# Kernel optimization log

Hardware: AMD Instinct MI355X
Metric: run time of the kernel (lower is better)

## Reference

```python
import jax, jax.numpy as jnp
import numpy as np

N_NODES = 40000
N_EDGES = 640000
N_FEAT = 128
HIDDEN = 128
N_GRAPHS = 64


def _sage_conv(x, src, dst, Wl, b, Wr):
    # PyG SAGEConv (aggr='mean', root_weight=True, normalize=False):
    # out_i = W_l @ mean_{j in N(i)} x_j + b + W_r @ x_i
    msg = x[src]                                             # [E, F]
    s = jax.ops.segment_sum(msg, dst, num_segments=N_NODES)  # [N, F]
    deg = jax.ops.segment_sum(jnp.ones((src.shape[0],), x.dtype), dst,
                              num_segments=N_NODES)
    agg = s / jnp.maximum(deg, 1.0)[:, None]
    return agg @ Wl + b + x @ Wr


def setup_inputs() -> dict:
    key = jax.random.key(0)
    ks = jax.random.split(key, 12)
    sc = 1.0 / np.sqrt(N_FEAT)
    x = jax.random.normal(ks[0], (N_NODES, N_FEAT), dtype=jnp.float32)
    edge_index = jax.random.randint(ks[1], (2, N_EDGES), 0, N_NODES, dtype=jnp.int32)
    batch = jnp.sort(jax.random.randint(ks[2], (N_NODES,), 0, N_GRAPHS, dtype=jnp.int32))
    mk = lambda k, shp: (jax.random.normal(k, shp, dtype=jnp.float32) * sc)
    return {
        'x': x, 'edge_index': edge_index, 'batch': batch,
        'W1l': mk(ks[3], (N_FEAT, HIDDEN)), 'b1': jnp.zeros((HIDDEN,), jnp.float32),
        'W1r': mk(ks[4], (N_FEAT, HIDDEN)),
        'W2l': mk(ks[5], (HIDDEN, HIDDEN)), 'b2': jnp.zeros((HIDDEN,), jnp.float32),
        'W2r': mk(ks[6], (HIDDEN, HIDDEN)),
        'W3l': mk(ks[7], (HIDDEN, HIDDEN)), 'b3': jnp.zeros((HIDDEN,), jnp.float32),
        'W3r': mk(ks[8], (HIDDEN, HIDDEN)),
        'Wlin': mk(ks[9], (3 * HIDDEN, HIDDEN)), 'blin': jnp.zeros((HIDDEN,), jnp.float32),
    }


def reference(x, edge_index, batch, W1l, b1, W1r, W2l, b2, W2r, W3l, b3, W3r, Wlin, blin):
    src, dst = edge_index[0], edge_index[1]
    h1 = jax.nn.relu(_sage_conv(x, src, dst, W1l, b1, W1r))
    h2 = jax.nn.relu(_sage_conv(h1, src, dst, W2l, b2, W2r))
    h3 = jax.nn.relu(_sage_conv(h2, src, dst, W3l, b3, W3r))
    h = jnp.concatenate([h1, h2, h3], axis=1)                # [N, 3*H]
    pooled = jax.ops.segment_sum(h, batch, num_segments=N_GRAPHS)  # global_add_pool
    out = jax.nn.relu(pooled @ Wlin + blin)                  # [G, H]
    return out
```

## Files before the change

### kernel.cpp

```cpp
#include <hip/hip_runtime.h>
#include <hip/hip_bf16.h>

#define N_NODES 40000
#define N_EDGES 640000
#define NFEAT 128
#define NGRAPHS 64
#define ECAP 1024

typedef __attribute__((ext_vector_type(8))) short short8;
typedef __attribute__((ext_vector_type(4))) float float4v;

static __device__ __forceinline__ float bf2f(unsigned short u) {
    unsigned int x = ((unsigned int)u) << 16;
    return __builtin_bit_cast(float, x);
}
static __device__ __forceinline__ unsigned short f2bf(float f) {
    unsigned int x = __builtin_bit_cast(unsigned int, f);
    unsigned int r = x + 0x7fffu + ((x >> 16) & 1u);
    return (unsigned short)(r >> 16);
}

__global__ void k_prep(const int* __restrict__ dst, int* __restrict__ deg,
                       const int* __restrict__ batch, int* __restrict__ goff,
                       const float* __restrict__ x, unsigned short* __restrict__ h0,
                       const float* __restrict__ Wl0, const float* __restrict__ Wr0,
                       const float* __restrict__ Wl1, const float* __restrict__ Wr1,
                       const float* __restrict__ Wl2, const float* __restrict__ Wr2,
                       unsigned short* __restrict__ Wt) {
    int b = blockIdx.x;
    if (b < 2500) {
        int e = b * 256 + threadIdx.x;
        if (e < N_EDGES) atomicAdd(&deg[dst[e]], 1);
    } else if (b < 2657) {
        int i = (b - 2500) * 256 + threadIdx.x;
        if (i >= N_NODES) return;
        int b1 = batch[i];
        int b0 = (i == 0) ? -1 : batch[i - 1];
        for (int g = b0 + 1; g <= b1; ++g) goff[g] = i;
        if (i == N_NODES - 1)
            for (int g = b1 + 1; g <= NGRAPHS; ++g) goff[g] = N_NODES;
    } else if (b < 12657) {
        int i = (b - 2657) * 256 + threadIdx.x;
        const int n = N_NODES * NFEAT / 2;
        if (i < n) {
            float a = x[2 * i], c = x[2 * i + 1];
            unsigned int u = (unsigned int)f2bf(a) | ((unsigned int)f2bf(c) << 16);
            ((unsigned int*)h0)[i] = u;
        }
    } else {
        int id = (b - 12657) * 256 + threadIdx.x;
        if (id >= 3 * 128 * 256) return;
        int l   = id >> 15;
        int rem = id & 32767;
        int nn  = rem >> 8;
        int k   = rem & 255;
        const float* Wl = (l == 0) ? Wl0 : (l == 1) ? Wl1 : Wl2;
        const float* Wr = (l == 0) ? Wr0 : (l == 1) ? Wr1 : Wr2;
        float v = (k < 128) ? Wl[k * 128 + nn] : Wr[(k - 128) * 128 + nn];
        Wt[id] = f2bf(v);
    }
}

__global__ __launch_bounds__(1024) void k_scan(const int* __restrict__ deg,
                                               int* __restrict__ offsets,
                                               int* __restrict__ cursor) {
    __shared__ int ws[16];
    __shared__ int s_boff;
    int tid = threadIdx.x;
    int b = blockIdx.x;
    int lane = tid & 63, wave = tid >> 6;

    int lim = b << 10;
    int s = 0;
    for (int i = tid; i < lim; i += 1024) s += deg[i];
    for (int d = 1; d < 64; d <<= 1) s += __shfl_xor(s, d, 64);
    if (lane == 0) ws[wave] = s;
    __syncthreads();
    if (tid == 0) {
        int t = 0;
        for (int w = 0; w < 16; ++w) t += ws[w];
        s_boff = t;
    }
    __syncthreads();
    int boff = s_boff;

    int i = (b << 10) + tid;
    int v = (i < N_NODES) ? deg[i] : 0;
    int incl = v;
    for (int d = 1; d < 64; d <<= 1) {
        int t = __shfl_up(incl, d, 64);
        if (lane >= d) incl += t;
    }
    __syncthreads();
    if (lane == 63) ws[wave] = incl;
    __syncthreads();
    if (wave == 0 && lane < 16) {
        int w = ws[lane];
        for (int d = 1; d < 16; d <<= 1) {
            int t = __shfl_up(w, d, 64);
            if (lane >= d) w += t;
        }
        ws[lane] = w;
    }
    __syncthreads();
    int waveOff = (wave == 0) ? 0 : ws[wave - 1];
    if (i < N_NODES) {
        int o = boff + waveOff + incl - v;
        offsets[i] = o;
        cursor[i]  = o;
    }
    if (b == 39 && tid == 0) offsets[N_NODES] = N_EDGES;
}

__global__ void k_fill(const int* __restrict__ src, const int* __restrict__ dst,
                       int* __restrict__ cursor, int* __restrict__ esrc) {
    int e = blockIdx.x * 256 + threadIdx.x;
    if (e < N_EDGES) {
        int d = dst[e];
        int p = atomicAdd(&cursor[d], 1);
        esrc[p] = src[e];
    }
}

__global__ __launch_bounds__(256, 7) void k_sage(
        const unsigned short* __restrict__ hin,
        const int* __restrict__ offsets,
        const int* __restrict__ esrc,
        const unsigned short* __restrict__ Wt,
        const float* __restrict__ bias,
        unsigned short* __restrict__ hout) {
    __shared__ __align__(16) unsigned short As[32][264];
    __shared__ int eidx[ECAP];
    int tid = threadIdx.x;
    int row0 = blockIdx.x * 32;

    int estart = offsets[row0];
    int ecnt   = offsets[row0 + 32] - estart;
    int staged = ecnt < ECAP ? ecnt : ECAP;

    for (int p = 0; p < 2; ++p) {
        int ci = tid + p * 256;
        int r = ci >> 4, c8 = ci & 15;
        uint4 v = *(const uint4*)(hin + (size_t)(row0 + r) * 128 + c8 * 8);
        *(uint4*)(&As[r][128 + c8 * 8]) = v;
    }
    for (int t = tid; t < staged; t += 256) eidx[t] = esrc[estart + t];
    __syncthreads();

    {
        int grp = tid >> 4;
        int sub = tid & 15;
        for (int nn = 0; nn < 2; ++nn) {
            int r = nn * 16 + grp;
            int node = row0 + r;
            int beg = offsets[node], end = offsets[node + 1];
            float a[8];
            for (int i = 0; i < 8; ++i) a[i] = 0.f;
            auto acc8 = [&](uint4 u) {
                a[0] += bf2f((unsigned short)(u.x & 0xffffu));
                a[1] += bf2f((unsigned short)(u.x >> 16));
                a[2] += bf2f((unsigned short)(u.y & 0xffffu));
                a[3] += bf2f((unsigned short)(u.y >> 16));
                a[4] += bf2f((unsigned short)(u.z & 0xffffu));
                a[5] += bf2f((unsigned short)(u.z >> 16));
                a[6] += bf2f((unsigned short)(u.w & 0xffffu));
                a[7] += bf2f((unsigned short)(u.w >> 16));
            };
            if (end - estart <= staged) {
                int lj = beg - estart, lend = end - estart;
                for (; lj + 8 <= lend; lj += 8) {
                    int s0 = eidx[lj],     s1 = eidx[lj + 1];
                    int s2 = eidx[lj + 2], s3 = eidx[lj + 3];
                    int s4 = eidx[lj + 4], s5 = eidx[lj + 5];
                    int s6 = eidx[lj + 6], s7 = eidx[lj + 7];
                    uint4 u0 = *(const uint4*)(hin + (size_t)s0 * 128 + sub * 8);
                    uint4 u1 = *(const uint4*)(hin + (size_t)s1 * 128 + sub * 8);
                    uint4 u2 = *(const uint4*)(hin + (size_t)s2 * 128 + sub * 8);
                    uint4 u3 = *(const uint4*)(hin + (size_t)s3 * 128 + sub * 8);
                    uint4 u4 = *(const uint4*)(hin + (size_t)s4 * 128 + sub * 8);
                    uint4 u5 = *(const uint4*)(hin + (size_t)s5 * 128 + sub * 8);
                    uint4 u6 = *(const uint4*)(hin + (size_t)s6 * 128 + sub * 8);
                    uint4 u7 = *(const uint4*)(hin + (size_t)s7 * 128 + sub * 8);
                    acc8(u0); acc8(u1); acc8(u2); acc8(u3);
                    acc8(u4); acc8(u5); acc8(u6); acc8(u7);
                }
                for (; lj < lend; ++lj) {
                    int s = eidx[lj];
                    uint4 u = *(const uint4*)(hin + (size_t)s * 128 + sub * 8);
                    acc8(u);
                }
            } else {
                for (int j = beg; j < end; ++j) {
                    int s = esrc[j];
                    uint4 u = *(const uint4*)(hin + (size_t)s * 128 + sub * 8);
                    acc8(u);
                }
            }
            int deg = end - beg;
            float inv = 1.f / (float)(deg > 1 ? deg : 1);
            uint4 v;
            v.x = (unsigned int)f2bf(a[0] * inv) | ((unsigned int)f2bf(a[1] * inv) << 16);
            v.y = (unsigned int)f2bf(a[2] * inv) | ((unsigned int)f2bf(a[3] * inv) << 16);
            v.z = (unsigned int)f2bf(a[4] * inv) | ((unsigned int)f2bf(a[5] * inv) << 16);
            v.w = (unsigned int)f2bf(a[6] * inv) | ((unsigned int)f2bf(a[7] * inv) << 16);
            *(uint4*)(&As[r][sub * 8]) = v;
        }
    }
    __syncthreads();

    int wave = tid >> 6, lane = tid & 63;
    int quad = lane >> 4, l16 = lane & 15;
    float4v acc[2][2];
    for (int rt = 0; rt < 2; ++rt)
        for (int ct = 0; ct < 2; ++ct) acc[rt][ct] = {0.f, 0.f, 0.f, 0.f};

    int ncol0 = wave * 32;
    for (int kc = 0; kc < 8; ++kc) {
        int k0 = kc * 32 + quad * 8;
        short8 a[2], b[2];
        for (int rt = 0; rt < 2; ++rt)
            a[rt] = *(const short8*)(&As[rt * 16 + l16][k0]);
        for (int ct = 0; ct < 2; ++ct)
            b[ct] = *(const short8*)(Wt + (size_t)(ncol0 + ct * 16 + l16) * 256 + k0);
        for (int rt = 0; rt < 2; ++rt)
            for (int ct = 0; ct < 2; ++ct)
                acc[rt][ct] = __builtin_amdgcn_mfma_f32_16x16x32_bf16(
                    a[rt], b[ct], acc[rt][ct], 0, 0, 0);
    }

    for (int ct = 0; ct < 2; ++ct) {
        int col = ncol0 + ct * 16 + l16;
        float bv = bias[col];
        for (int rt = 0; rt < 2; ++rt) {
            int r0 = rt * 16 + quad * 4;
            for (int i = 0; i < 4; ++i) {
                float v = acc[rt][ct][i] + bv;
                v = v > 0.f ? v : 0.f;
                hout[(size_t)(row0 + r0 + i) * 128 + col] = f2bf(v);
            }
        }
    }
}

__global__ __launch_bounds__(256) void k_pool(const unsigned short* __restrict__ h1,
                                              const unsigned short* __restrict__ h2,
                                              const unsigned short* __restrict__ h3,
                                              const int* __restrict__ goff,
                                              float* __restrict__ pooled) {
    __shared__ float red[4][16][8];
    int b = blockIdx.x;
    int g = b / 3, aidx = b % 3;
    const unsigned short* h = (aidx == 0) ? h1 : (aidx == 1) ? h2 : h3;
    int beg = goff[g], end = goff[g + 1];
    int tid = threadIdx.x;
    int rp = tid >> 4;
    int ch = tid & 15;
    float a[8];
    for (int i = 0; i < 8; ++i) a[i] = 0.f;
    for (int r = beg + rp; r < end; r += 16) {
        uint4 u = *(const uint4*)(h + (size_t)r * 128 + ch * 8);
        a[0] += bf2f((unsigned short)(u.x & 0xffffu));
        a[1] += bf2f((unsigned short)(u.x >> 16));
        a[2] += bf2f((unsigned short)(u.y & 0xffffu));
        a[3] += bf2f((unsigned short)(u.y >> 16));
        a[4] += bf2f((unsigned short)(u.z & 0xffffu));
        a[5] += bf2f((unsigned short)(u.z >> 16));
        a[6] += bf2f((unsigned short)(u.w & 0xffffu));
        a[7] += bf2f((unsigned short)(u.w >> 16));
    }
    for (int i = 0; i < 8; ++i) {
        a[i] += __shfl_xor(a[i], 16, 64);
        a[i] += __shfl_xor(a[i], 32, 64);
    }
    int wave = tid >> 6, lane = tid & 63;
    if (lane < 16)
        for (int i = 0; i < 8; ++i) red[wave][lane][i] = a[i];
    __syncthreads();
    if (tid < 128) {
        int ch2 = tid >> 3, e = tid & 7;
        float s = red[0][ch2][e] + red[1][ch2][e] + red[2][ch2][e] + red[3][ch2][e];
        pooled[g * 384 + aidx * 128 + ch2 * 8 + e] = s;
    }
}

__global__ void k_final(const float* __restrict__ pooled,
                        const float* __restrict__ Wlin,
                        const float* __restrict__ blin,
                        float* __restrict__ out) {
    int g = blockIdx.x, col = threadIdx.x;
    float acc = blin[col];
    for (int k = 0; k < 384; ++k)
        acc = fmaf(pooled[g * 384 + k], Wlin[k * 128 + col], acc);
    out[g * 128 + col] = acc > 0.f ? acc : 0.f;
}

extern "C" void kernel_launch(void* const* d_in, const int* in_sizes, int n_in,
                              void* d_out, int out_size, void* d_ws, size_t ws_size,
                              hipStream_t stream) {
    const float* x    = (const float*)d_in[0];
    const int*   ei   = (const int*)d_in[1];
    const int*   src  = ei;
    const int*   dst  = ei + N_EDGES;
    const int*   batch = (const int*)d_in[2];
    const float* W1l = (const float*)d_in[3];
    const float* b1  = (const float*)d_in[4];
    const float* W1r = (const float*)d_in[5];
    const float* W2l = (const float*)d_in[6];
    const float* b2  = (const float*)d_in[7];
    const float* W2r = (const float*)d_in[8];
    const float* W3l = (const float*)d_in[9];
    const float* b3  = (const float*)d_in[10];
    const float* W3r = (const float*)d_in[11];
    const float* Wlin = (const float*)d_in[12];
    const float* blin = (const float*)d_in[13];
    float* out = (float*)d_out;

    char* ws = (char*)d_ws;
    size_t off = 0;
    auto alloc = [&](size_t bytes) -> char* {
        char* p = ws + off;
        off = (off + bytes + 255) & ~(size_t)255;
        return p;
    };
    int* offsets = (int*)alloc((N_NODES + 1) * sizeof(int));
    int* cursor  = (int*)alloc(N_NODES * sizeof(int));
    int* deg     = (int*)alloc(N_NODES * sizeof(int));
    int* goff    = (int*)alloc((NGRAPHS + 1) * sizeof(int));
    int* esrc    = (int*)alloc(N_EDGES * sizeof(int));
    unsigned short* h0   = (unsigned short*)alloc((size_t)N_NODES * 128 * 2);
    unsigned short* h1   = (unsigned short*)alloc((size_t)N_NODES * 128 * 2);
    unsigned short* h2   = (unsigned short*)alloc((size_t)N_NODES * 128 * 2);
    unsigned short* h3   = (unsigned short*)alloc((size_t)N_NODES * 128 * 2);
    unsigned short* Wt   = (unsigned short*)alloc(3 * 256 * 128 * 2);
    float* pooled = (float*)alloc(NGRAPHS * 384 * sizeof(float));

    hipMemsetAsync(deg, 0, N_NODES * sizeof(int), stream);

    k_prep<<<13041, 256, 0, stream>>>(dst, deg, batch, goff, x, h0,
                                      W1l, W1r, W2l, W2r, W3l, W3r, Wt);
    k_scan<<<40, 1024, 0, stream>>>(deg, offsets, cursor);
    k_fill<<<(N_EDGES + 255) / 256, 256, 0, stream>>>(src, dst, cursor, esrc);

    k_sage<<<1250, 256, 0, stream>>>(h0, offsets, esrc, Wt,             b1, h1);
    k_sage<<<1250, 256, 0, stream>>>(h1, offsets, esrc, Wt + 32768,     b2, h2);
    k_sage<<<1250, 256, 0, stream>>>(h2, offsets, esrc, Wt + 2 * 32768, b3, h3);

    k_pool<<<3 * NGRAPHS, 256, 0, stream>>>(h1, h2, h3, goff, pooled);
    k_final<<<NGRAPHS, 128, 0, stream>>>(pooled, Wlin, blin, out);
}
```

Measured before the change: 274.5 us.

## Split neighbor gather across edge lanes with shuffle reduction in SAGE kernel

The aggregation loop used to give each of the 16 lanes per node a fixed 8-column slice, with every lane walking all edges of its node. Now each lane group of 4 walks a strided quarter of the edges, cycling over 4 column chunks, and combines partial sums with xor-shuffles. The aim is more independent gather loads in flight and less serial edge-loop latency per lane. The edge staging buffer is reduced and the occupancy hint raised to 8 blocks per CU, at the cost of extra shuffle work, repeated eidx reads per column chunk, and more fallback to the global edge path.

```diff
diff --git a/kernel.cpp b/kernel.cpp
--- a/kernel.cpp
+++ b/kernel.cpp
@@ -5,7 +5,7 @@
 #define N_EDGES 640000
 #define NFEAT 128
 #define NGRAPHS 64
-#define ECAP 1024
+#define ECAP 768
 
 typedef __attribute__((ext_vector_type(8))) short short8;
 typedef __attribute__((ext_vector_type(4))) float float4v;
@@ -122,7 +122,7 @@
     }
 }
 
-__global__ __launch_bounds__(256, 7) void k_sage(
+__global__ __launch_bounds__(256, 8) void k_sage(
         const unsigned short* __restrict__ hin,
         const int* __restrict__ offsets,
         const int* __restrict__ esrc,
@@ -149,61 +149,69 @@
 
     {
         int grp = tid >> 4;
-        int sub = tid & 15;
+        int l   = tid & 15;
+        int e4  = l >> 2;
+        int q4  = l & 3;
         for (int nn = 0; nn < 2; ++nn) {
             int r = nn * 16 + grp;
             int node = row0 + r;
             int beg = offsets[node], end = offsets[node + 1];
-            float a[8];
-            for (int i = 0; i < 8; ++i) a[i] = 0.f;
-            auto acc8 = [&](uint4 u) {
-                a[0] += bf2f((unsigned short)(u.x & 0xffffu));
-                a[1] += bf2f((unsigned short)(u.x >> 16));
-                a[2] += bf2f((unsigned short)(u.y & 0xffffu));
-                a[3] += bf2f((unsigned short)(u.y >> 16));
-                a[4] += bf2f((unsigned short)(u.z & 0xffffu));
-                a[5] += bf2f((unsigned short)(u.z >> 16));
-                a[6] += bf2f((unsigned short)(u.w & 0xffffu));
-                a[7] += bf2f((unsigned short)(u.w >> 16));
-            };
-            if (end - estart <= staged) {
-                int lj = beg - estart, lend = end - estart;
-                for (; lj + 8 <= lend; lj += 8) {
-                    int s0 = eidx[lj],     s1 = eidx[lj + 1];
-                    int s2 = eidx[lj + 2], s3 = eidx[lj + 3];
-                    int s4 = eidx[lj + 4], s5 = eidx[lj + 5];
-                    int s6 = eidx[lj + 6], s7 = eidx[lj + 7];
-                    uint4 u0 = *(const uint4*)(hin + (size_t)s0 * 128 + sub * 8);
-                    uint4 u1 = *(const uint4*)(hin + (size_t)s1 * 128 + sub * 8);
-                    uint4 u2 = *(const uint4*)(hin + (size_t)s2 * 128 + sub * 8);
-                    uint4 u3 = *(const uint4*)(hin + (size_t)s3 * 128 + sub * 8);
-                    uint4 u4 = *(const uint4*)(hin + (size_t)s4 * 128 + sub * 8);
-                    uint4 u5 = *(const uint4*)(hin + (size_t)s5 * 128 + sub * 8);
-                    uint4 u6 = *(const uint4*)(hin + (size_t)s6 * 128 + sub * 8);
-                    uint4 u7 = *(const uint4*)(hin + (size_t)s7 * 128 + sub * 8);
-                    acc8(u0); acc8(u1); acc8(u2); acc8(u3);
-                    acc8(u4); acc8(u5); acc8(u6); acc8(u7);
+            int deg = end - beg;
+            float inv = 1.f / (float)(deg > 1 ? deg : 1);
+            bool fast = (end - estart <= staged);
+            int lend = end - estart;
+            int lbeg = beg - estart;
+
+            for (int p = 0; p < 4; ++p) {
+                int co = (p * 4 + q4) * 8;
+                float a[8];
+                for (int i = 0; i < 8; ++i) a[i] = 0.f;
+                auto acc8 = [&](uint4 u) {
+                    a[0] += bf2f((unsigned short)(u.x & 0xffffu));
+                    a[1] += bf2f((unsigned short)(u.x >> 16));
+                    a[2] += bf2f((unsigned short)(u.y & 0xffffu));
+                    a[3] += bf2f((unsigned short)(u.y >> 16));
+                    a[4] += bf2f((unsigned short)(u.z & 0xffffu));
+                    a[5] += bf2f((unsigned short)(u.z >> 16));
+                    a[6] += bf2f((unsigned short)(u.w & 0xffffu));
+                    a[7] += bf2f((unsigned short)(u.w >> 16));
+                };
+                if (fast) {
+                    int lj = lbeg + e4;
+                    for (; lj + 12 < lend; lj += 16) {
+                        int s0 = eidx[lj], s1 = eidx[lj + 4];
+                        int s2 = eidx[lj + 8], s3 = eidx[lj + 12];
+                        uint4 u0 = *(const uint4*)(hin + (size_t)s0 * 128 + co);
+                        uint4 u1 = *(const uint4*)(hin + (size_t)s1 * 128 + co);
+                        uint4 u2 = *(const uint4*)(hin + (size_t)s2 * 128 + co);
+                        uint4 u3 = *(const uint4*)(hin + (size_t)s3 * 128 + co);
+                        acc8(u0); acc8(u1); acc8(u2); acc8(u3);
+                    }
+                    for (; lj < lend; lj += 4) {
+                        int s = eidx[lj];
+                        uint4 u = *(const uint4*)(hin + (size_t)s * 128 + co);
+                        acc8(u);
+                    }
+                } else {
+                    for (int j = beg + e4; j < end; j += 4) {
+                        int s = esrc[j];
+                        uint4 u = *(const uint4*)(hin + (size_t)s * 128 + co);
+                        acc8(u);
+                    }
                 }
-                for (; lj < lend; ++lj) {
-                    int s = eidx[lj];
-                    uint4 u = *(const uint4*)(hin + (size_t)s * 128 + sub * 8);
-                    acc8(u);
+                for (int i = 0; i < 8; ++i) {
+                    a[i] += __shfl_xor(a[i], 4, 64);
+                    a[i] += __shfl_xor(a[i], 8, 64);
                 }
-            } else {
-                for (int j = beg; j < end; ++j) {
-                    int s = esrc[j];
-                    uint4 u = *(const uint4*)(hin + (size_t)s * 128 + sub * 8);
-                    acc8(u);
+                if (e4 == 0) {
+                    uint4 v;
+                    v.x = (unsigned int)f2bf(a[0] * inv) | ((unsigned int)f2bf(a[1] * inv) << 16);
+                    v.y = (unsigned int)f2bf(a[2] * inv) | ((unsigned int)f2bf(a[3] * inv) << 16);
+                    v.z = (unsigned int)f2bf(a[4] * inv) | ((unsigned int)f2bf(a[5] * inv) << 16);
+                    v.w = (unsigned int)f2bf(a[6] * inv) | ((unsigned int)f2bf(a[7] * inv) << 16);
+                    *(uint4*)(&As[r][co]) = v;
                 }
             }
-            int deg = end - beg;
-            float inv = 1.f / (float)(deg > 1 ? deg : 1);
-            uint4 v;
-            v.x = (unsigned int)f2bf(a[0] * inv) | ((unsigned int)f2bf(a[1] * inv) << 16);
-            v.y = (unsigned int)f2bf(a[2] * inv) | ((unsigned int)f2bf(a[3] * inv) << 16);
-            v.z = (unsigned int)f2bf(a[4] * inv) | ((unsigned int)f2bf(a[5] * inv) << 16);
-            v.w = (unsigned int)f2bf(a[6] * inv) | ((unsigned int)f2bf(a[7] * inv) << 16);
-            *(uint4*)(&As[r][sub * 8]) = v;
         }
     }
     __syncthreads();
```

Result: slower. 309.2 us (+12.7%).
